# Optimization experiments

Hardware: AMD Instinct MI355X
Metric: run time of the kernel (lower is better)

## Reference

```python
import jax, jax.numpy as jnp
import numpy as np

S, N, H, AD, AR = 256, 1024, 512, 128, 2

def setup_inputs() -> dict:
    key = jax.random.key(0)
    k0, k1, k2, k3, k4, k5 = jax.random.split(key, 6)
    xav1 = np.sqrt(2.0 / (H + AD)).astype(np.float32)   # xavier_normal std for [H,AD]
    xav2 = np.sqrt(2.0 / (AD + AR)).astype(np.float32)  # xavier_normal std for [AD,AR]
    return {
        "pre_emb_padded": jax.random.normal(k0, (S, N, H), jnp.float32),
        "fol_emb_padded": jax.random.normal(k1, (S, N, H), jnp.float32),
        "pre_attn_mask": jnp.zeros((N, S), jnp.bool_),
        "fol_attn_mask": jnp.zeros((N, S), jnp.bool_),
        "pre_is_valid": jnp.ones((N,), jnp.int32),
        "fol_is_valid": jnp.ones((N,), jnp.int32),
        "W1_pre": jax.random.normal(k2, (H, AD), jnp.float32) * xav1,
        "W2_pre": jax.random.normal(k3, (AD, AR), jnp.float32) * xav2,
        "W1_fol": jax.random.normal(k4, (H, AD), jnp.float32) * xav1,
        "W2_fol": jax.random.normal(k5, (AD, AR), jnp.float32) * xav2,
    }

def _attn_pool(emb, mask, W1, W2):
    # emb: [S, N, H] -> x: [N, S, H]
    x = jnp.transpose(emb, (1, 0, 2))
    s = jnp.tanh(x @ W1) @ W2                 # [N, S, 2]
    s = jax.nn.softmax(s, axis=1)             # softmax over seq (first softmax)
    s = jnp.transpose(s, (0, 2, 1))           # [N, 2, S]
    s = jnp.where(mask[:, None, :], -jnp.inf, s)
    s = jax.nn.softmax(s, axis=-1)            # masked second softmax over seq
    return jnp.einsum('nrs,nsh->nrh', s, x)   # [N, 2, H]

def _scatter_valid(h, valid):
    # reproduce the python valid-list gather: valid rows take next chunk, else zeros
    pos = jnp.cumsum(valid) - 1               # [N]
    return jnp.where((valid > 0)[:, None, None], h[pos], jnp.zeros((), h.dtype))

def reference(pre_emb_padded, fol_emb_padded, pre_attn_mask, fol_attn_mask,
              pre_is_valid, fol_is_valid, W1_pre, W2_pre, W1_fol, W2_fol):
    h_pre = _scatter_valid(_attn_pool(pre_emb_padded, pre_attn_mask, W1_pre, W2_pre), pre_is_valid)
    h_fol = _scatter_valid(_attn_pool(fol_emb_padded, fol_attn_mask, W1_fol, W2_fol), fol_is_valid)
    # mean over the attn_r=2 rows, concat along feature dim -> [N, 1, 2H]
    return jnp.concatenate([h_pre.mean(axis=1, keepdims=True),
                            h_fol.mean(axis=1, keepdims=True)], axis=2)
```

## Files before the change

### kernel.cpp

```cpp
#include <hip/hip_runtime.h>
#include <hip/hip_bf16.h>
#include <cstdint>
#include <cstddef>

#define S_ 256
#define N_ 1024
#define H_ 512
#define AD_ 128
static constexpr int M_TOTAL = N_ * S_;

typedef __attribute__((ext_vector_type(8))) short short8;
typedef __attribute__((ext_vector_type(4))) float f32x4;

#define LDS_BARRIER()                                       \
  asm volatile("s_waitcnt lgkmcnt(0)" ::: "memory");        \
  __builtin_amdgcn_s_barrier()

__device__ __forceinline__ float red16_dpp(float v) {
  union fi { float f; int i; };
  fi a, r;
  a.f = v;
  r.i = __builtin_amdgcn_update_dpp(0, a.i, 0xB1, 0xF, 0xF, true);
  a.f += r.f;
  r.i = __builtin_amdgcn_update_dpp(0, a.i, 0x4E, 0xF, 0xF, true);
  a.f += r.f;
  r.i = __builtin_amdgcn_update_dpp(0, a.i, 0x124, 0xF, 0xF, true);
  a.f += r.f;
  r.i = __builtin_amdgcn_update_dpp(0, a.i, 0x128, 0xF, 0xF, true);
  a.f += r.f;
  return a.f;
}

__global__ __launch_bounds__(256) void k_w1frag(
    const float* __restrict__ w1_pre, const float* __restrict__ w1_fol,
    unsigned short* __restrict__ w1f) {
  int idx = blockIdx.x * 256 + threadIdx.x;
  int st = blockIdx.y;
  const float* w1 = st ? w1_fol : w1_pre;
  int j = idx & 7;
  int lane = (idx >> 3) & 63;
  int c = (idx >> 9) & 7;
  int kk = idx >> 12;
  int k = kk * 32 + ((lane >> 4) << 3) + j;
  int d = c * 16 + (lane & 15);
  __hip_bfloat16 hb = __float2bfloat16(w1[(size_t)k * AD_ + d]);
  w1f[(size_t)st * 65536 + idx] = *(unsigned short*)&hb;
}

__global__ __launch_bounds__(1024) void k_scan(
    const int* __restrict__ valid_pre, const int* __restrict__ valid_fol,
    int* __restrict__ pos) {
  const int st = blockIdx.x;
  const int* valid = st ? valid_fol : valid_pre;
  __shared__ int buf[1024];
  const int t = threadIdx.x;
  buf[t] = valid[t];
  __syncthreads();
  for (int off = 1; off < 1024; off <<= 1) {
    int v = (t >= off) ? buf[t - off] : 0;
    __syncthreads();
    buf[t] += v;
    __syncthreads();
  }
  pos[st * N_ + t] = buf[t] - 1;
}

__global__ __launch_bounds__(512) void k_fused(
    const float* __restrict__ emb_pre, const float* __restrict__ emb_fol,
    const unsigned short* __restrict__ w1f,
    const float* __restrict__ w2_pre, const float* __restrict__ w2_fol,
    const unsigned char* __restrict__ mask_pre, const unsigned char* __restrict__ mask_fol,
    float* __restrict__ part) {
  __shared__ __align__(16) unsigned char As[32768];
  __shared__ float partb[2][8][16][2];
  __shared__ float lgbuf[S_][2];
  __shared__ float wl[S_];
  __shared__ __align__(16) float p3[4][128][4];
  __shared__ float pad_[9216];

  const int t = threadIdx.x;
  if (blockDim.y == 2) pad_[t] = 0.f;

  const int bid = blockIdx.x;
  const int st  = bid >> 10;
  const int n   = bid & 1023;
  const float* __restrict__ emb = st ? emb_fol : emb_pre;
  const float* __restrict__ w2  = st ? w2_fol : w2_pre;
  const unsigned char* __restrict__ mask = st ? mask_fol : mask_pre;

  const int w = t >> 6, lane = t & 63;
  const int r16 = lane & 15, kq = lane >> 4;

  short8 B[16];
  {
    const unsigned short* bb = w1f + (size_t)st * 65536 + w * 512 + (size_t)lane * 8;
#pragma unroll
    for (int kk = 0; kk < 16; ++kk) B[kk] = *(const short8*)(bb + kk * 4096);
  }
  const float w2v0 = w2[(w * 16 + r16) * 2 + 0];
  const float w2v1 = w2[(w * 16 + r16) * 2 + 1];

  const size_t SSTR = (size_t)N_ * H_;
  const float* baseA = emb + ((size_t)w * N_ + n) * H_;
  unsigned wadr[4];
#pragma unroll
  for (int j = 0; j < 4; ++j) {
    int cb = (j & 1) * 1024 + lane * 16;
    int R  = (j >> 1) * 8 + w;
    int g16 = cb >> 5, half = (cb >> 4) & 1;
    wadr[j] = (unsigned)(R * 1024 + ((g16 ^ (R & 7)) * 16) + half * 8);
  }

  float4 nxt[4];
#define LD_STEP(MS)                                                          \
  {                                                                          \
    _Pragma("unroll")                                                        \
    for (int j = 0; j < 4; ++j)                                              \
      nxt[j] = *(const float4*)(baseA + (size_t)(MS) * 16 * SSTR +           \
                                (size_t)(j >> 1) * 8 * SSTR +                \
                                (j & 1) * 256 + lane * 4);                   \
  }
#define ST_STEP(BUFB)                                                        \
  {                                                                          \
    _Pragma("unroll")                                                        \
    for (int j = 0; j < 4; ++j) {                                            \
      union { unsigned long long u; __hip_bfloat162 h[2]; } p;               \
      p.h[0] = __float22bfloat162_rn(make_float2(nxt[j].x, nxt[j].y));       \
      p.h[1] = __float22bfloat162_rn(make_float2(nxt[j].z, nxt[j].w));       \
      *(unsigned long long*)&As[(BUFB) + wadr[j]] = p.u;                     \
    }                                                                        \
  }

  LD_STEP(0);
  ST_STEP(0);
  LD_STEP(1);
  LDS_BARRIER();

  for (int ss = 0; ss < 16; ++ss) {
    const int cur = ss & 1;
    const int nb  = cur ^ 1;
    const unsigned abase = (unsigned)(cur << 14);

    if (ss < 15) ST_STEP((unsigned)(nb << 14));
    if (ss < 14) LD_STEP(ss + 2);

    if (ss > 0 && lane < 4) {
      int vv = w * 4 + lane;
      int row = vv >> 1, rr = vv & 1;
      float v = 0.f;
#pragma unroll
      for (int g = 0; g < 8; ++g) v += partb[nb][g][row][rr];
      lgbuf[(ss - 1) * 16 + row][rr] = v;
    }

    f32x4 a0 = (f32x4){0.f, 0.f, 0.f, 0.f};
    f32x4 a1 = (f32x4){0.f, 0.f, 0.f, 0.f};
#pragma unroll
    for (int kk = 0; kk < 16; ++kk) {
      const unsigned ra = abase +
          (unsigned)(r16 * 1024 + (((kk * 4 + kq) ^ (r16 & 7)) * 16));
      short8 a = *(const short8*)&As[ra];
      if (kk & 1)
        a1 = __builtin_amdgcn_mfma_f32_16x16x32_bf16(a, B[kk], a1, 0, 0, 0);
      else
        a0 = __builtin_amdgcn_mfma_f32_16x16x32_bf16(a, B[kk], a0, 0, 0, 0);
    }

#pragma unroll
    for (int q = 0; q < 4; ++q) {
      float xc = fminf(fmaxf(a0[q] + a1[q], -10.f), 10.f);
      float e  = __expf(2.f * xc);
      float th = (e - 1.f) / (e + 1.f);
      float p0 = red16_dpp(th * w2v0);
      float p1 = red16_dpp(th * w2v1);
      if (r16 == 0) {
        partb[cur][w][kq * 4 + q][0] = p0;
        partb[cur][w][kq * 4 + q][1] = p1;
      }
    }
    LDS_BARRIER();
  }

  if (lane < 4) {
    int vv = w * 4 + lane;
    int row = vv >> 1, rr = vv & 1;
    float v = 0.f;
#pragma unroll
    for (int g = 0; g < 8; ++g) v += partb[1][g][row][rr];
    lgbuf[240 + row][rr] = v;
  }
  LDS_BARRIER();

  if (w == 0) {
    uchar4 mkb = *(const uchar4*)(mask + (size_t)n * S_ + lane * 4);
    float l0[4], l1[4];
    bool mk[4];
#pragma unroll
    for (int i = 0; i < 4; ++i) {
      l0[i] = lgbuf[lane * 4 + i][0];
      l1[i] = lgbuf[lane * 4 + i][1];
    }
    mk[0] = mkb.x != 0; mk[1] = mkb.y != 0; mk[2] = mkb.z != 0; mk[3] = mkb.w != 0;
    float q0[4], q1[4];
#pragma unroll
    for (int r = 0; r < 2; ++r) {
      float* lv = r ? l1 : l0;
      float* qq = r ? q1 : q0;
      float m1 = fmaxf(fmaxf(lv[0], lv[1]), fmaxf(lv[2], lv[3]));
#pragma unroll
      for (int off = 32; off; off >>= 1) m1 = fmaxf(m1, __shfl_xor(m1, off));
      float e[4], s1 = 0.f;
#pragma unroll
      for (int i = 0; i < 4; ++i) { e[i] = __expf(lv[i] - m1); s1 += e[i]; }
#pragma unroll
      for (int off = 32; off; off >>= 1) s1 += __shfl_xor(s1, off);
      float inv1 = 1.f / s1;
      float v[4];
#pragma unroll
      for (int i = 0; i < 4; ++i) v[i] = mk[i] ? -INFINITY : e[i] * inv1;
      float m2 = fmaxf(fmaxf(v[0], v[1]), fmaxf(v[2], v[3]));
#pragma unroll
      for (int off = 32; off; off >>= 1) m2 = fmaxf(m2, __shfl_xor(m2, off));
      float e2[4], s2 = 0.f;
#pragma unroll
      for (int i = 0; i < 4; ++i) { e2[i] = mk[i] ? 0.f : __expf(v[i] - m2); s2 += e2[i]; }
#pragma unroll
      for (int off = 32; off; off >>= 1) s2 += __shfl_xor(s2, off);
      float inv2 = 1.f / s2;
#pragma unroll
      for (int i = 0; i < 4; ++i) qq[i] = e2[i] * inv2;
    }
#pragma unroll
    for (int i = 0; i < 4; ++i) wl[lane * 4 + i] = 0.5f * (q0[i] + q1[i]);
  }
  LDS_BARRIER();

  {
    const int sg = t >> 7, tt = t & 127, c0 = tt * 4;
    const float* embn = emb + (size_t)n * H_ + c0;
    float4 acc = (float4){0.f, 0.f, 0.f, 0.f};
    const int sTop = sg * 64 + 63;
#pragma unroll
    for (int b2 = 0; b2 < 8; ++b2) {
      const int sb = sTop - b2 * 8;
      float4 x[8];
#pragma unroll
      for (int i = 0; i < 8; ++i)
        x[i] = *(const float4*)(embn + (size_t)(sb - i) * SSTR);
#pragma unroll
      for (int i = 0; i < 8; ++i) {
        const float wv = wl[sb - i];
        acc.x += wv * x[i].x;
        acc.y += wv * x[i].y;
        acc.z += wv * x[i].z;
        acc.w += wv * x[i].w;
      }
    }
    *(float4*)&p3[sg][tt][0] = acc;
  }
  LDS_BARRIER();
  if (t < 128) {
    float4 r;
    r.x = p3[0][t][0] + p3[1][t][0] + p3[2][t][0] + p3[3][t][0];
    r.y = p3[0][t][1] + p3[1][t][1] + p3[2][t][1] + p3[3][t][1];
    r.z = p3[0][t][2] + p3[1][t][2] + p3[2][t][2] + p3[3][t][2];
    r.w = p3[0][t][3] + p3[1][t][3] + p3[2][t][3] + p3[3][t][3];
    *(float4*)&part[((size_t)st * N_ + n) * H_ + t * 4] = r;
  }
}

__global__ __launch_bounds__(256) void k_combine(
    const float* __restrict__ part, const int* __restrict__ pos,
    const int* __restrict__ valid_pre, const int* __restrict__ valid_fol,
    float* __restrict__ out) {
  const int n = blockIdx.x, t = threadIdx.x;
  const int st = t >> 7;
  const int c = (t & 127) * 4;
  const int* valid = st ? valid_fol : valid_pre;
  float4 r = {0.f, 0.f, 0.f, 0.f};
  if (valid[n] > 0) {
    int np = pos[st * N_ + n]; if (np < 0) np = 0;
    r = *(const float4*)&part[((size_t)st * N_ + np) * H_ + c];
  }
  *(float4*)&out[(size_t)n * 1024 + st * 512 + c] = r;
}

extern "C" void kernel_launch(void* const* d_in, const int* in_sizes, int n_in,
                              void* d_out, int out_size, void* d_ws, size_t ws_size,
                              hipStream_t stream) {
  const float* emb_pre = (const float*)d_in[0];
  const float* emb_fol = (const float*)d_in[1];
  const unsigned char* mask_pre = (const unsigned char*)d_in[2];
  const unsigned char* mask_fol = (const unsigned char*)d_in[3];
  const int* valid_pre = (const int*)d_in[4];
  const int* valid_fol = (const int*)d_in[5];
  const float* w1_pre = (const float*)d_in[6];
  const float* w2_pre = (const float*)d_in[7];
  const float* w1_fol = (const float*)d_in[8];
  const float* w2_fol = (const float*)d_in[9];
  float* out = (float*)d_out;

  char* ws = (char*)d_ws;
  unsigned short* w1f = (unsigned short*)ws;
  int*   pos    = (int*)(ws + 262144);
  float* part   = (float*)(ws + 270336);

  hipLaunchKernelGGL(k_w1frag, dim3(256, 2), dim3(256), 0, stream,
                     w1_pre, w1_fol, w1f);
  hipLaunchKernelGGL(k_scan, dim3(2), dim3(1024), 0, stream,
                     valid_pre, valid_fol, pos);
  hipLaunchKernelGGL(k_fused, dim3(2048), dim3(512), 0, stream,
                     emb_pre, emb_fol, w1f, w2_pre, w2_fol,
                     mask_pre, mask_fol, part);
  hipLaunchKernelGGL(k_combine, dim3(N_), dim3(256), 0, stream,
                     part, pos, valid_pre, valid_fol, out);
}
```

Before: 383.9 us.

## Persistent blocks overlapping the next row's score GEMM with the previous row's pooling

Measured after the change: 422.0 us. 1.1x slower.

```diff
diff --git a/kernel.cpp b/kernel.cpp
--- a/kernel.cpp
+++ b/kernel.cpp
@@ -76,32 +76,13 @@
   __shared__ float lgbuf[S_][2];
   __shared__ float wl[S_];
   __shared__ __align__(16) float p3[4][128][4];
-  __shared__ float pad_[9216];
-
+
+  const int b = blockIdx.x;
   const int t = threadIdx.x;
-  if (blockDim.y == 2) pad_[t] = 0.f;
-
-  const int bid = blockIdx.x;
-  const int st  = bid >> 10;
-  const int n   = bid & 1023;
-  const float* __restrict__ emb = st ? emb_fol : emb_pre;
-  const float* __restrict__ w2  = st ? w2_fol : w2_pre;
-  const unsigned char* __restrict__ mask = st ? mask_fol : mask_pre;
-
   const int w = t >> 6, lane = t & 63;
   const int r16 = lane & 15, kq = lane >> 4;
-
-  short8 B[16];
-  {
-    const unsigned short* bb = w1f + (size_t)st * 65536 + w * 512 + (size_t)lane * 8;
-#pragma unroll
-    for (int kk = 0; kk < 16; ++kk) B[kk] = *(const short8*)(bb + kk * 4096);
-  }
-  const float w2v0 = w2[(w * 16 + r16) * 2 + 0];
-  const float w2v1 = w2[(w * 16 + r16) * 2 + 1];
-
   const size_t SSTR = (size_t)N_ * H_;
-  const float* baseA = emb + ((size_t)w * N_ + n) * H_;
+
   unsigned wadr[4];
 #pragma unroll
   for (int j = 0; j < 4; ++j) {
@@ -110,8 +91,11 @@
     int g16 = cb >> 5, half = (cb >> 4) & 1;
     wadr[j] = (unsigned)(R * 1024 + ((g16 ^ (R & 7)) * 16) + half * 8);
   }
+  const int sg = t >> 7, tt = t & 127, c0b = tt * 4;
 
   float4 nxt[4];
+  const float* baseA = emb_pre;
+
 #define LD_STEP(MS)                                                          \
   {                                                                          \
     _Pragma("unroll")                                                        \
@@ -131,142 +115,173 @@
     }                                                                        \
   }
 
-  LD_STEP(0);
-  ST_STEP(0);
-  LD_STEP(1);
-  LDS_BARRIER();
-
-  for (int ss = 0; ss < 16; ++ss) {
-    const int cur = ss & 1;
-    const int nb  = cur ^ 1;
-    const unsigned abase = (unsigned)(cur << 14);
-
-    if (ss < 15) ST_STEP((unsigned)(nb << 14));
-    if (ss < 14) LD_STEP(ss + 2);
-
-    if (ss > 0 && lane < 4) {
+  short8 B[16];
+  float w2v0 = 0.f, w2v1 = 0.f;
+  float4 accv = (float4){0.f, 0.f, 0.f, 0.f};
+  const float* prevEmbN = emb_pre;
+  float* prevPart = part;
+
+  for (int jp = 0; jp < 9; ++jp) {
+    const bool do_p1 = (jp < 8), do_pv = (jp > 0);
+    const int st = (jp >> 2) & 1;
+    const int n  = b + (jp & 3) * 256;
+    const float* __restrict__ emb = st ? emb_fol : emb_pre;
+    const unsigned char* __restrict__ mask = st ? mask_fol : mask_pre;
+    const float* __restrict__ w2 = st ? w2_fol : w2_pre;
+
+    if (do_p1) {
+      baseA = emb + ((size_t)w * N_ + n) * H_;
+      const unsigned short* bb =
+          w1f + (size_t)st * 65536 + w * 512 + (size_t)lane * 8;
+#pragma unroll
+      for (int kk = 0; kk < 16; ++kk) B[kk] = *(const short8*)(bb + kk * 4096);
+      w2v0 = w2[(w * 16 + r16) * 2 + 0];
+      w2v1 = w2[(w * 16 + r16) * 2 + 1];
+      LD_STEP(0);
+      ST_STEP(0);
+      LD_STEP(1);
+    }
+    LDS_BARRIER();
+
+    for (int ss = 0; ss < 16; ++ss) {
+      const int cur = ss & 1;
+      const int nb  = cur ^ 1;
+      const unsigned abase = (unsigned)(cur << 14);
+
+      if (do_p1 && ss < 15) ST_STEP((unsigned)(nb << 14));
+
+      float4 xv0, xv1, xv2, xv3;
+      if (do_pv) {
+        const float* pb = prevEmbN + (size_t)(ss * 16 + sg * 4) * SSTR + c0b;
+        xv0 = *(const float4*)(pb);
+        xv1 = *(const float4*)(pb + SSTR);
+        xv2 = *(const float4*)(pb + 2 * SSTR);
+        xv3 = *(const float4*)(pb + 3 * SSTR);
+      }
+      __builtin_amdgcn_sched_barrier(0);
+      if (do_p1 && ss < 14) LD_STEP(ss + 2);
+
+      if (do_p1 && ss > 0 && lane < 4) {
+        int vv = w * 4 + lane;
+        int row = vv >> 1, rr = vv & 1;
+        float v = 0.f;
+#pragma unroll
+        for (int g = 0; g < 8; ++g) v += partb[nb][g][row][rr];
+        lgbuf[(ss - 1) * 16 + row][rr] = v;
+      }
+
+      if (do_p1) {
+        f32x4 a0 = (f32x4){0.f, 0.f, 0.f, 0.f};
+        f32x4 a1 = (f32x4){0.f, 0.f, 0.f, 0.f};
+#pragma unroll
+        for (int kk = 0; kk < 16; ++kk) {
+          const unsigned ra = abase +
+              (unsigned)(r16 * 1024 + (((kk * 4 + kq) ^ (r16 & 7)) * 16));
+          short8 a = *(const short8*)&As[ra];
+          if (kk & 1)
+            a1 = __builtin_amdgcn_mfma_f32_16x16x32_bf16(a, B[kk], a1, 0, 0, 0);
+          else
+            a0 = __builtin_amdgcn_mfma_f32_16x16x32_bf16(a, B[kk], a0, 0, 0, 0);
+        }
+#pragma unroll
+        for (int q = 0; q < 4; ++q) {
+          float xc = fminf(fmaxf(a0[q] + a1[q], -10.f), 10.f);
+          float e  = __expf(2.f * xc);
+          float th = (e - 1.f) / (e + 1.f);
+          float p0 = red16_dpp(th * w2v0);
+          float p1 = red16_dpp(th * w2v1);
+          if (r16 == 0) {
+            partb[cur][w][kq * 4 + q][0] = p0;
+            partb[cur][w][kq * 4 + q][1] = p1;
+          }
+        }
+      }
+
+      if (do_pv) {
+        const int s0v = ss * 16 + sg * 4;
+        float w0 = wl[s0v], w1v = wl[s0v + 1], w2w = wl[s0v + 2], w3 = wl[s0v + 3];
+        accv.x += w0 * xv0.x + w1v * xv1.x + w2w * xv2.x + w3 * xv3.x;
+        accv.y += w0 * xv0.y + w1v * xv1.y + w2w * xv2.y + w3 * xv3.y;
+        accv.z += w0 * xv0.z + w1v * xv1.z + w2w * xv2.z + w3 * xv3.z;
+        accv.w += w0 * xv0.w + w1v * xv1.w + w2w * xv2.w + w3 * xv3.w;
+      }
+      LDS_BARRIER();
+    }
+
+    if (do_p1 && lane < 4) {
       int vv = w * 4 + lane;
       int row = vv >> 1, rr = vv & 1;
       float v = 0.f;
 #pragma unroll
-      for (int g = 0; g < 8; ++g) v += partb[nb][g][row][rr];
-      lgbuf[(ss - 1) * 16 + row][rr] = v;
-    }
-
-    f32x4 a0 = (f32x4){0.f, 0.f, 0.f, 0.f};
-    f32x4 a1 = (f32x4){0.f, 0.f, 0.f, 0.f};
-#pragma unroll
-    for (int kk = 0; kk < 16; ++kk) {
-      const unsigned ra = abase +
-          (unsigned)(r16 * 1024 + (((kk * 4 + kq) ^ (r16 & 7)) * 16));
-      short8 a = *(const short8*)&As[ra];
-      if (kk & 1)
-        a1 = __builtin_amdgcn_mfma_f32_16x16x32_bf16(a, B[kk], a1, 0, 0, 0);
-      else
-        a0 = __builtin_amdgcn_mfma_f32_16x16x32_bf16(a, B[kk], a0, 0, 0, 0);
-    }
-
-#pragma unroll
-    for (int q = 0; q < 4; ++q) {
-      float xc = fminf(fmaxf(a0[q] + a1[q], -10.f), 10.f);
-      float e  = __expf(2.f * xc);
-      float th = (e - 1.f) / (e + 1.f);
-      float p0 = red16_dpp(th * w2v0);
-      float p1 = red16_dpp(th * w2v1);
-      if (r16 == 0) {
-        partb[cur][w][kq * 4 + q][0] = p0;
-        partb[cur][w][kq * 4 + q][1] = p1;
-      }
-    }
+      for (int g = 0; g < 8; ++g) v += partb[1][g][row][rr];
+      lgbuf[240 + row][rr] = v;
+    }
+    if (do_pv) *(float4*)&p3[sg][tt][0] = accv;
     LDS_BARRIER();
-  }
-
-  if (lane < 4) {
-    int vv = w * 4 + lane;
-    int row = vv >> 1, rr = vv & 1;
-    float v = 0.f;
-#pragma unroll
-    for (int g = 0; g < 8; ++g) v += partb[1][g][row][rr];
-    lgbuf[240 + row][rr] = v;
-  }
-  LDS_BARRIER();
-
-  if (w == 0) {
-    uchar4 mkb = *(const uchar4*)(mask + (size_t)n * S_ + lane * 4);
-    float l0[4], l1[4];
-    bool mk[4];
-#pragma unroll
-    for (int i = 0; i < 4; ++i) {
-      l0[i] = lgbuf[lane * 4 + i][0];
-      l1[i] = lgbuf[lane * 4 + i][1];
-    }
-    mk[0] = mkb.x != 0; mk[1] = mkb.y != 0; mk[2] = mkb.z != 0; mk[3] = mkb.w != 0;
-    float q0[4], q1[4];
-#pragma unroll
-    for (int r = 0; r < 2; ++r) {
-      float* lv = r ? l1 : l0;
-      float* qq = r ? q1 : q0;
-      float m1 = fmaxf(fmaxf(lv[0], lv[1]), fmaxf(lv[2], lv[3]));
-#pragma unroll
-      for (int off = 32; off; off >>= 1) m1 = fmaxf(m1, __shfl_xor(m1, off));
-      float e[4], s1 = 0.f;
-#pragma unroll
-      for (int i = 0; i < 4; ++i) { e[i] = __expf(lv[i] - m1); s1 += e[i]; }
-#pragma unroll
-      for (int off = 32; off; off >>= 1) s1 += __shfl_xor(s1, off);
-      float inv1 = 1.f / s1;
-      float v[4];
-#pragma unroll
-      for (int i = 0; i < 4; ++i) v[i] = mk[i] ? -INFINITY : e[i] * inv1;
-      float m2 = fmaxf(fmaxf(v[0], v[1]), fmaxf(v[2], v[3]));
-#pragma unroll
-      for (int off = 32; off; off >>= 1) m2 = fmaxf(m2, __shfl_xor(m2, off));
-      float e2[4], s2 = 0.f;
-#pragma unroll
-      for (int i = 0; i < 4; ++i) { e2[i] = mk[i] ? 0.f : __expf(v[i] - m2); s2 += e2[i]; }
-#pragma unroll
-      for (int off = 32; off; off >>= 1) s2 += __shfl_xor(s2, off);
-      float inv2 = 1.f / s2;
-#pragma unroll
-      for (int i = 0; i < 4; ++i) qq[i] = e2[i] * inv2;
-    }
-#pragma unroll
-    for (int i = 0; i < 4; ++i) wl[lane * 4 + i] = 0.5f * (q0[i] + q1[i]);
-  }
-  LDS_BARRIER();
-
-  {
-    const int sg = t >> 7, tt = t & 127, c0 = tt * 4;
-    const float* embn = emb + (size_t)n * H_ + c0;
-    float4 acc = (float4){0.f, 0.f, 0.f, 0.f};
-    const int sTop = sg * 64 + 63;
-#pragma unroll
-    for (int b2 = 0; b2 < 8; ++b2) {
-      const int sb = sTop - b2 * 8;
-      float4 x[8];
-#pragma unroll
-      for (int i = 0; i < 8; ++i)
-        x[i] = *(const float4*)(embn + (size_t)(sb - i) * SSTR);
-#pragma unroll
-      for (int i = 0; i < 8; ++i) {
-        const float wv = wl[sb - i];
-        acc.x += wv * x[i].x;
-        acc.y += wv * x[i].y;
-        acc.z += wv * x[i].z;
-        acc.w += wv * x[i].w;
-      }
-    }
-    *(float4*)&p3[sg][tt][0] = acc;
-  }
-  LDS_BARRIER();
-  if (t < 128) {
-    float4 r;
-    r.x = p3[0][t][0] + p3[1][t][0] + p3[2][t][0] + p3[3][t][0];
-    r.y = p3[0][t][1] + p3[1][t][1] + p3[2][t][1] + p3[3][t][1];
-    r.z = p3[0][t][2] + p3[1][t][2] + p3[2][t][2] + p3[3][t][2];
-    r.w = p3[0][t][3] + p3[1][t][3] + p3[2][t][3] + p3[3][t][3];
-    *(float4*)&part[((size_t)st * N_ + n) * H_ + t * 4] = r;
-  }
+
+    if (do_pv && t < 128) {
+      float4 r;
+      r.x = p3[0][t][0] + p3[1][t][0] + p3[2][t][0] + p3[3][t][0];
+      r.y = p3[0][t][1] + p3[1][t][1] + p3[2][t][1] + p3[3][t][1];
+      r.z = p3[0][t][2] + p3[1][t][2] + p3[2][t][2] + p3[3][t][2];
+      r.w = p3[0][t][3] + p3[1][t][3] + p3[2][t][3] + p3[3][t][3];
+      *(float4*)&prevPart[t * 4] = r;
+    }
+
+    if (do_p1 && w == 0) {
+      uchar4 mkb = *(const uchar4*)(mask + (size_t)n * S_ + lane * 4);
+      float l0[4], l1[4];
+      bool mk[4];
+#pragma unroll
+      for (int i = 0; i < 4; ++i) {
+        l0[i] = lgbuf[lane * 4 + i][0];
+        l1[i] = lgbuf[lane * 4 + i][1];
+      }
+      mk[0] = mkb.x != 0; mk[1] = mkb.y != 0;
+      mk[2] = mkb.z != 0; mk[3] = mkb.w != 0;
+      float q0[4], q1[4];
+#pragma unroll
+      for (int r = 0; r < 2; ++r) {
+        float* lv = r ? l1 : l0;
+        float* qq = r ? q1 : q0;
+        float m1 = fmaxf(fmaxf(lv[0], lv[1]), fmaxf(lv[2], lv[3]));
+#pragma unroll
+        for (int off = 32; off; off >>= 1) m1 = fmaxf(m1, __shfl_xor(m1, off));
+        float e[4], s1 = 0.f;
+#pragma unroll
+        for (int i = 0; i < 4; ++i) { e[i] = __expf(lv[i] - m1); s1 += e[i]; }
+#pragma unroll
+        for (int off = 32; off; off >>= 1) s1 += __shfl_xor(s1, off);
+        float inv1 = 1.f / s1;
+        float v[4];
+#pragma unroll
+        for (int i = 0; i < 4; ++i) v[i] = mk[i] ? -INFINITY : e[i] * inv1;
+        float m2 = fmaxf(fmaxf(v[0], v[1]), fmaxf(v[2], v[3]));
+#pragma unroll
+        for (int off = 32; off; off >>= 1) m2 = fmaxf(m2, __shfl_xor(m2, off));
+        float e2[4], s2 = 0.f;
+#pragma unroll
+        for (int i = 0; i < 4; ++i) {
+          e2[i] = mk[i] ? 0.f : __expf(v[i] - m2);
+          s2 += e2[i];
+        }
+#pragma unroll
+        for (int off = 32; off; off >>= 1) s2 += __shfl_xor(s2, off);
+        float inv2 = 1.f / s2;
+#pragma unroll
+        for (int i = 0; i < 4; ++i) qq[i] = e2[i] * inv2;
+      }
+#pragma unroll
+      for (int i = 0; i < 4; ++i) wl[lane * 4 + i] = 0.5f * (q0[i] + q1[i]);
+    }
+    LDS_BARRIER();
+
+    prevEmbN = emb + (size_t)n * H_;
+    prevPart = part + ((size_t)st * N_ + n) * H_;
+    accv = (float4){0.f, 0.f, 0.f, 0.f};
+  }
+#undef LD_STEP
+#undef ST_STEP
 }
 
 __global__ __launch_bounds__(256) void k_combine(
@@ -309,7 +324,7 @@
                      w1_pre, w1_fol, w1f);
   hipLaunchKernelGGL(k_scan, dim3(2), dim3(1024), 0, stream,
                      valid_pre, valid_fol, pos);
-  hipLaunchKernelGGL(k_fused, dim3(2048), dim3(512), 0, stream,
+  hipLaunchKernelGGL(k_fused, dim3(256), dim3(512), 0, stream,
                      emb_pre, emb_fol, w1f, w2_pre, w2_fol,
                      mask_pre, mask_fol, part);
   hipLaunchKernelGGL(k_combine, dim3(N_), dim3(256), 0, stream,
```
